# Kernel optimization log

Measured on AMD Instinct MI355X. Metric: run time of the kernel, lower is better.

The kernel has to match this reference:

```python
import jax, jax.numpy as jnp
import numpy as np

K_SIZE = 5  # neighborhood window

def _extract_patches(x, k):
    # tf.image.extract_patches with stride 1, SAME (zero) padding.
    # x: [B,H,W,C] -> [B,H,W,k*k,C]
    pad = k // 2
    B, H, W, C = x.shape
    xp = jnp.pad(x, ((0, 0), (pad, pad), (pad, pad), (0, 0)))
    # fixed small k*k loop (25 shifted views), stacked along patch axis
    return jnp.stack([xp[:, i:i + H, j:j + W, :]
                      for i in range(k) for j in range(k)], axis=3)

def setup_inputs() -> dict:
    key = jax.random.key(0)
    k1, k2, k3 = jax.random.split(key, 3)
    B, H, W, C, BIN = 2, 256, 256, 32, 32
    return {
        "main": jax.random.normal(k1, (B, H, W, C), dtype=jnp.float32),
        "ref": jax.random.normal(k2, (B, H, W, C), dtype=jnp.float32),
        "ref_value": jax.random.normal(k3, (B, H, W, BIN), dtype=jnp.float32),
    }

def reference(main, ref, ref_value):
    # mode='dot': local-window dot-product attention
    ref_stacked = _extract_patches(ref, K_SIZE)          # [B,H,W,k*k,C]
    attn = jnp.einsum('bhwc,bhwkc->bhwk', main, ref_stacked)
    attn = jax.nn.softmax(attn, axis=-1)                 # [B,H,W,k*k]
    # aggregate_mode='weighted_sum'
    ref_value_stacked = _extract_patches(ref_value, K_SIZE)  # [B,H,W,k*k,bin]
    return jnp.einsum('bhwk,bhwki->bhwi', attn, ref_value_stacked)
```

## Files before the change

### kernel.cpp

```cpp
#include <hip/hip_runtime.h>


#define STRIP 2

__global__ void __launch_bounds__(256)
local_attn_kernel(const float* __restrict__ main_p,
                  const float* __restrict__ ref_p,
                  const float* __restrict__ rv_p,
                  float* __restrict__ out_p)
{
    const int tid  = threadIdx.x;
    const int lane = tid & 63;
    const int wv   = tid >> 6;
    const int cg   = lane & 7;
    const int pw   = lane >> 3;

    const int bid = blockIdx.x;
    const int cb  = bid & 7;
    const int rb  = (bid >> 3) & 127;
    const int b   = bid >> 10;

    const int w   = cb * 32 + wv * 8 + pw;
    const int hb  = rb * STRIP;
    const int ib  = b << 16;

    const float4* m4 = (const float4*)main_p;
    const float4* r4 = (const float4*)ref_p;
    const float4* v4 = (const float4*)rv_p;
    float4*       o4 = (float4*)out_p;

    int   cbase[5];
    float cmask[5];
#pragma unroll
    for (int j = 0; j < 5; ++j) {
        const int wj = w + j - 2;
        cmask[j] = ((unsigned)wj < 256u) ? 1.0f : 0.0f;
        const int wc = min(max(wj, 0), 255);
        cbase[j] = ((ib + wc) << 3) + cg;
    }

    const float L2E = 1.44269504088896340736f;

    float4 m[STRIP];
    float4 acc[STRIP];
    float  sum[STRIP];
#pragma unroll
    for (int k = 0; k < STRIP; ++k) {
        const float4 t = m4[((ib + (hb + k) * 256 + w) << 3) + cg];
        m[k]   = make_float4(t.x * L2E, t.y * L2E, t.z * L2E, t.w * L2E);
        acc[k] = make_float4(0.f, 0.f, 0.f, 0.f);
        sum[k] = 0.0f;
    }

#pragma unroll 1
    for (int rr = 0; rr < STRIP + 4; ++rr) {
        const int   r    = hb + rr - 2;
        const float rok  = ((unsigned)r < 256u) ? 1.0f : 0.0f;
        const int   roff = min(max(r, 0), 255) << 11;

        float wm[STRIP];
#pragma unroll
        for (int k = 0; k < STRIP; ++k)
            wm[k] = (k <= rr && rr <= k + 4) ? 1.0f : 0.0f;

#pragma unroll
        for (int j = 0; j < 5; ++j) {
            const int    a   = cbase[j] + roff;
            const float4 rr4 = r4[a];
            const float4 vv4 = v4[a];
            const float  mj  = cmask[j] * rok;

#pragma unroll
            for (int k = 0; k < STRIP; ++k) {
                float s = m[k].x * rr4.x + m[k].y * rr4.y
                        + m[k].z * rr4.z + m[k].w * rr4.w;
                s += __shfl_xor(s, 1, 64);
                s += __shfl_xor(s, 2, 64);
                s += __shfl_xor(s, 4, 64);

                const float e  = __builtin_exp2f(s * mj);
                const float ew = e * wm[k];
                sum[k] += ew;
                const float t = ew * mj;
                acc[k].x += t * vv4.x;
                acc[k].y += t * vv4.y;
                acc[k].z += t * vv4.z;
                acc[k].w += t * vv4.w;
            }
        }
    }

#pragma unroll
    for (int k = 0; k < STRIP; ++k) {
        const float inv = 1.0f / sum[k];
        float4 o;
        o.x = acc[k].x * inv; o.y = acc[k].y * inv;
        o.z = acc[k].z * inv; o.w = acc[k].w * inv;
        o4[((ib + (hb + k) * 256 + w) << 3) + cg] = o;
    }
}

extern "C" void kernel_launch(void* const* d_in, const int* in_sizes, int n_in,
                              void* d_out, int out_size, void* d_ws, size_t ws_size,
                              hipStream_t stream)
{
    const float* main_p = (const float*)d_in[0];
    const float* ref_p  = (const float*)d_in[1];
    const float* rv_p   = (const float*)d_in[2];
    float*       out_p  = (float*)d_out;

    const int npix   = in_sizes[0] / 32;
    const int blocks = npix / (32 * STRIP);
    local_attn_kernel<<<blocks, 256, 0, stream>>>(main_p, ref_p, rv_p, out_p);
}
```

Before: 106.2 us.

## Stage ref and value rows through double-buffered shared memory

Each block cooperatively loads one row of ref and ref_value (32 columns plus a 4-column halo, 576 float4s) into LDS, then reads the five horizontal neighbors from LDS instead of issuing five global loads per thread. Loads for the next row are issued before computing on the current row and written to the alternate buffer afterward, which overlaps global latency with compute. The aim is to cut redundant global/L2 traffic from the horizontal window. The cost is an added barrier per row and more LDS use per block.

```diff
diff --git a/kernel.cpp b/kernel.cpp
--- a/kernel.cpp
+++ b/kernel.cpp
@@ -20,24 +20,36 @@
     const int rb  = (bid >> 3) & 127;
     const int b   = bid >> 10;
 
-    const int w   = cb * 32 + wv * 8 + pw;
-    const int hb  = rb * STRIP;
-    const int ib  = b << 16;
+    const int w    = cb * 32 + wv * 8 + pw;
+    const int col0 = cb * 32;
+    const int hb   = rb * STRIP;
+    const int ib   = b << 16;
 
     const float4* m4 = (const float4*)main_p;
     const float4* r4 = (const float4*)ref_p;
     const float4* v4 = (const float4*)rv_p;
     float4*       o4 = (float4*)out_p;
 
-    int   cbase[5];
+    __shared__ float4 smem[2 * 576];
+
+    const float4* sp[3];
+    const int nchunk = (tid < 64) ? 3 : 2;
+#pragma unroll
+    for (int ps = 0; ps < 3; ++ps) {
+        int c = tid + (ps << 8);
+        if (c > 575) c = 575;
+        const int isrv = (c >= 288);
+        const int cc   = isrv ? c - 288 : c;
+        const int col  = cc >> 3;
+        const int cgc  = cc & 7;
+        const int colg = min(max(col0 - 2 + col, 0), 255);
+        sp[ps] = (isrv ? v4 : r4) + (((ib + colg) << 3) + cgc);
+    }
+
     float cmask[5];
 #pragma unroll
-    for (int j = 0; j < 5; ++j) {
-        const int wj = w + j - 2;
-        cmask[j] = ((unsigned)wj < 256u) ? 1.0f : 0.0f;
-        const int wc = min(max(wj, 0), 255);
-        cbase[j] = ((ib + wc) << 3) + cg;
-    }
+    for (int j = 0; j < 5; ++j)
+        cmask[j] = ((unsigned)(w + j - 2) < 256u) ? 1.0f : 0.0f;
 
     const float L2E = 1.44269504088896340736f;
 
@@ -52,12 +64,35 @@
         sum[k] = 0.0f;
     }
 
+    const int lbase = ((wv * 8 + pw) << 3) + cg;
+
+    {
+        const int roff = (min(max(hb - 2, 0), 255)) << 11;
+        float4 st0, st1, st2;
+        st0 = sp[0][roff];
+        st1 = sp[1][roff];
+        if (nchunk == 3) st2 = sp[2][roff];
+        smem[tid]       = st0;
+        smem[tid + 256] = st1;
+        if (nchunk == 3) smem[tid + 512] = st2;
+    }
+    __syncthreads();
+
 #pragma unroll 1
     for (int rr = 0; rr < STRIP + 4; ++rr) {
-        const int   r    = hb + rr - 2;
-        const float rok  = ((unsigned)r < 256u) ? 1.0f : 0.0f;
-        const int   roff = min(max(r, 0), 255) << 11;
+        const int   r   = hb + rr - 2;
+        const float rok = ((unsigned)r < 256u) ? 1.0f : 0.0f;
 
+        float4 st0, st1, st2;
+        const bool more = (rr < STRIP + 3);
+        if (more) {
+            const int roff = (min(max(hb + rr - 1, 0), 255)) << 11;
+            st0 = sp[0][roff];
+            st1 = sp[1][roff];
+            if (nchunk == 3) st2 = sp[2][roff];
+        }
+
+        const int bufb = (rr & 1) * 576;
         float wm[STRIP];
 #pragma unroll
         for (int k = 0; k < STRIP; ++k)
@@ -65,9 +100,8 @@
 
 #pragma unroll
         for (int j = 0; j < 5; ++j) {
-            const int    a   = cbase[j] + roff;
-            const float4 rr4 = r4[a];
-            const float4 vv4 = v4[a];
+            const float4 rr4 = smem[bufb + lbase + j * 8];
+            const float4 vv4 = smem[bufb + 288 + lbase + j * 8];
             const float  mj  = cmask[j] * rok;
 
 #pragma unroll
@@ -87,6 +121,14 @@
                 acc[k].z += t * vv4.z;
                 acc[k].w += t * vv4.w;
             }
+        }
+
+        if (more) {
+            const int nb = ((rr + 1) & 1) * 576;
+            smem[nb + tid]       = st0;
+            smem[nb + tid + 256] = st1;
+            if (nchunk == 3) smem[nb + tid + 512] = st2;
+            __syncthreads();
         }
     }
 
```

New measurement: 110.4 us. 3.9% more time.

## Stage ref/value rows in double-buffered LDS, use DPP reductions, skip masked rows

Applied to the files above, without the earlier changes.

Each block now loads one row of ref and ref_value (32+4 halo columns) cooperatively into a double-buffered shared-memory tile. All threads read their 5 column neighbours from LDS instead of issuing redundant global loads, and the next row's global loads are issued while the current row is computed. The 8-lane shuffle reduction is replaced with DPP row moves, and compile-time flags skip the strip rows that fall outside the window instead of multiplying by a zero weight. This adds barriers and LDS traffic per row, plus more complex unrolled control flow.

```diff
diff --git a/kernel.cpp b/kernel.cpp
--- a/kernel.cpp
+++ b/kernel.cpp
@@ -2,6 +2,13 @@
 
 
 #define STRIP 2
+
+template <int CTRL>
+__device__ __forceinline__ float dpp_add(float x)
+{
+    const int y = __builtin_amdgcn_mov_dpp(__float_as_int(x), CTRL, 0xF, 0xF, true);
+    return x + __int_as_float(y);
+}
 
 __global__ void __launch_bounds__(256)
 local_attn_kernel(const float* __restrict__ main_p,
@@ -20,24 +27,37 @@
     const int rb  = (bid >> 3) & 127;
     const int b   = bid >> 10;
 
-    const int w   = cb * 32 + wv * 8 + pw;
-    const int hb  = rb * STRIP;
-    const int ib  = b << 16;
+    const int w    = cb * 32 + wv * 8 + pw;
+    const int col0 = cb * 32;
+    const int hb   = rb * STRIP;
+    const int ib   = b << 16;
 
     const float4* m4 = (const float4*)main_p;
     const float4* r4 = (const float4*)ref_p;
     const float4* v4 = (const float4*)rv_p;
     float4*       o4 = (float4*)out_p;
 
-    int   cbase[5];
+    __shared__ float4 smem[2 * 576];
+
+    const bool has3 = (tid < 64);
+    const float4 *sp0, *sp1, *sp2;
+    {
+        const int c1 = tid + 256;
+        const int cc1 = (c1 < 288) ? c1 : c1 - 288;
+        const int c2 = (has3 ? tid + 512 : 575) - 288;
+
+        const int col0g0 = min(max(col0 - 2 + (tid >> 3), 0), 255);
+        const int col0g1 = min(max(col0 - 2 + (cc1 >> 3), 0), 255);
+        const int col0g2 = min(max(col0 - 2 + (c2  >> 3), 0), 255);
+        sp0 = r4 + (((ib + col0g0) << 3) + (tid & 7));
+        sp1 = ((c1 < 288) ? r4 : v4) + (((ib + col0g1) << 3) + (cc1 & 7));
+        sp2 = v4 + (((ib + col0g2) << 3) + (c2 & 7));
+    }
+
     float cmask[5];
 #pragma unroll
-    for (int j = 0; j < 5; ++j) {
-        const int wj = w + j - 2;
-        cmask[j] = ((unsigned)wj < 256u) ? 1.0f : 0.0f;
-        const int wc = min(max(wj, 0), 255);
-        cbase[j] = ((ib + wc) << 3) + cg;
-    }
+    for (int j = 0; j < 5; ++j)
+        cmask[j] = ((unsigned)(w + j - 2) < 256u) ? 1.0f : 0.0f;
 
     const float L2E = 1.44269504088896340736f;
 
@@ -52,43 +72,79 @@
         sum[k] = 0.0f;
     }
 
+    const int lbase = ((wv * 8 + pw) << 3) + cg;
+
+#define ISSUE(RRI, d0, d1, d2)                                              \
+    {                                                                        \
+        const int roff = (min(max(hb + (RRI) - 2, 0), 255)) << 11;           \
+        d0 = sp0[roff];                                                      \
+        d1 = sp1[roff];                                                      \
+        if (has3) d2 = sp2[roff];                                            \
+    }
+
+#define WRITE(BUFB, s0, s1, s2)                                              \
+    {                                                                        \
+        smem[(BUFB) + tid]       = s0;                                       \
+        smem[(BUFB) + tid + 256] = s1;                                       \
+        if (has3) smem[(BUFB) + tid + 512] = s2;                             \
+    }
+
+#define BODY(K)                                                              \
+    {                                                                        \
+        float s = m[K].x * rr4.x + m[K].y * rr4.y                            \
+                + m[K].z * rr4.z + m[K].w * rr4.w;                           \
+        s = dpp_add<0xB1>(s);                        \
+        s = dpp_add<0x4E>(s);                        \
+        s = dpp_add<0x141>(s);              \
+        const float e = __builtin_exp2f(s * mj);   \
+        sum[K] += e;                                                         \
+        const float t = e * mj;                    \
+        acc[K].x += t * vv4.x; acc[K].y += t * vv4.y;                        \
+        acc[K].z += t * vv4.z; acc[K].w += t * vv4.w;                        \
+    }
+
+#define COMPUTE(RR, BUFB, DOK0, DOK1)                                        \
+    {                                                                        \
+        const int   rI  = hb + (RR) - 2;                                     \
+        const float rok = ((unsigned)rI < 256u) ? 1.0f : 0.0f;               \
+        _Pragma("unroll")                                                    \
+        for (int j = 0; j < 5; ++j) {                                        \
+            const float4 rr4 = smem[(BUFB) + lbase + j * 8];                 \
+            const float4 vv4 = smem[(BUFB) + 288 + lbase + j * 8];           \
+            const float  mj  = cmask[j] * rok;                               \
+            if (DOK0) BODY(0)                                                \
+            if (DOK1) BODY(1)                                                \
+        }                                                                    \
+    }
+
+    float4 a0, a1, a2, b0, b1, b2;
+
+    ISSUE(0, a0, a1, a2);
+    WRITE(0, a0, a1, a2);
+    ISSUE(1, b0, b1, b2);
+    __syncthreads();
+
+    ISSUE(2, a0, a1, a2);
+    COMPUTE(0, 0, 1, 0);
+    WRITE(576, b0, b1, b2);
+    __syncthreads();
+
 #pragma unroll 1
-    for (int rr = 0; rr < STRIP + 4; ++rr) {
-        const int   r    = hb + rr - 2;
-        const float rok  = ((unsigned)r < 256u) ? 1.0f : 0.0f;
-        const int   roff = min(max(r, 0), 255) << 11;
+    for (int rr2 = 0; rr2 < 2; ++rr2) {
+        const int rrA = 2 * rr2 + 1;
+        ISSUE(rrA + 2, b0, b1, b2);
+        COMPUTE(rrA, (rrA & 1) * 576, 1, 1);
+        WRITE(((rrA + 1) & 1) * 576, a0, a1, a2);
+        __syncthreads();
 
-        float wm[STRIP];
-#pragma unroll
-        for (int k = 0; k < STRIP; ++k)
-            wm[k] = (k <= rr && rr <= k + 4) ? 1.0f : 0.0f;
+        const int rrB = rrA + 1;
+        if (rr2 == 0) ISSUE(rrB + 2, a0, a1, a2);
+        COMPUTE(rrB, (rrB & 1) * 576, 1, 1);
+        WRITE(((rrB + 1) & 1) * 576, b0, b1, b2);
+        __syncthreads();
+    }
 
-#pragma unroll
-        for (int j = 0; j < 5; ++j) {
-            const int    a   = cbase[j] + roff;
-            const float4 rr4 = r4[a];
-            const float4 vv4 = v4[a];
-            const float  mj  = cmask[j] * rok;
-
-#pragma unroll
-            for (int k = 0; k < STRIP; ++k) {
-                float s = m[k].x * rr4.x + m[k].y * rr4.y
-                        + m[k].z * rr4.z + m[k].w * rr4.w;
-                s += __shfl_xor(s, 1, 64);
-                s += __shfl_xor(s, 2, 64);
-                s += __shfl_xor(s, 4, 64);
-
-                const float e  = __builtin_exp2f(s * mj);
-                const float ew = e * wm[k];
-                sum[k] += ew;
-                const float t = ew * mj;
-                acc[k].x += t * vv4.x;
-                acc[k].y += t * vv4.y;
-                acc[k].z += t * vv4.z;
-                acc[k].w += t * vv4.w;
-            }
-        }
-    }
+    COMPUTE(5, 576, 0, 1);
 
 #pragma unroll
     for (int k = 0; k < STRIP; ++k) {
@@ -98,6 +154,11 @@
         o.z = acc[k].z * inv; o.w = acc[k].w * inv;
         o4[((ib + (hb + k) * 256 + w) << 3) + cg] = o;
     }
+
+#undef ISSUE
+#undef WRITE
+#undef BODY
+#undef COMPUTE
 }
 
 extern "C" void kernel_launch(void* const* d_in, const int* in_sizes, int n_in,
```

New measurement: 102.6 us. -3.4%, faster.
